# Optimization experiments

Hardware: AMD Instinct MI355X
Metric: run time of the kernel (lower is better)

Reference implementation:

```python
import jax, jax.numpy as jnp
import numpy as np

D_MODEL = 768
D_FF = 3072
N_EXPERTS = 4
BATCH, SEQ = 8, 2048


def setup_inputs() -> dict:
    key = jax.random.key(0)
    ks = jax.random.split(key, 8)
    s_in = 1.0 / np.sqrt(D_MODEL)
    s_ff = 1.0 / np.sqrt(D_FF)
    return {
        "hidden_states": jax.random.normal(ks[0], (BATCH, SEQ, D_MODEL), jnp.float32),
        "Wg": jax.random.normal(ks[1], (D_MODEL, N_EXPERTS), jnp.float32) * s_in,
        "bg": jnp.zeros((N_EXPERTS,), jnp.float32),
        "W1": jax.random.normal(ks[2], (N_EXPERTS, D_MODEL, D_FF), jnp.float32) * s_in,
        "b1": jnp.zeros((N_EXPERTS, D_FF), jnp.float32),
        "W2": jax.random.normal(ks[3], (N_EXPERTS, D_FF, D_MODEL), jnp.float32) * s_ff,
        "b2": jnp.zeros((N_EXPERTS, D_MODEL), jnp.float32),
    }


def reference(hidden_states, Wg, bg, W1, b1, W2, b2):
    """Switch-Transformer top-1 MoE FFN (no token dropping).

    router: softmax(x @ Wg + bg); each token goes to argmax expert,
    expert FFN: gelu(x @ W1[e] + b1[e]) @ W2[e] + b2[e],
    output scaled by the winning route probability.
    """
    B, S, D = hidden_states.shape
    xt = hidden_states.reshape(-1, D)                      # [T, D]
    logits = xt @ Wg + bg                                  # [T, E]
    probs = jax.nn.softmax(logits, axis=-1)
    gate = jnp.max(probs, axis=-1)                         # [T]
    route = jnp.argmax(probs, axis=-1)                     # [T] int

    out = jnp.zeros_like(xt)
    for e in range(W1.shape[0]):                           # small fixed expert count
        mask = (route == e).astype(xt.dtype)[:, None]      # [T, 1]
        h = jax.nn.gelu(xt @ W1[e] + b1[e])                # [T, d_ff]
        y = h @ W2[e] + b2[e]                              # [T, D]
        out = out + mask * y
    out = out * gate[:, None]
    return out.reshape(B, S, D)
```

## Files before the change

### kernel.cpp

```cpp
#include <hip/hip_runtime.h>
#include <hip/hip_bf16.h>

#define T_TOK 16384
#define DMODEL 768
#define DFF 3072
#define NEXP 4
#define ROWPAD 512
#define BK 64

typedef __attribute__((ext_vector_type(8))) short bf16x8;
typedef __attribute__((ext_vector_type(4))) float f32x4;

__device__ __forceinline__ void gl_lds16(const void* g, void* l) {
  __builtin_amdgcn_global_load_lds(
      (const __attribute__((address_space(1))) unsigned int*)g,
      (__attribute__((address_space(3))) unsigned int*)l, 16, 0, 0);
}

__device__ __forceinline__ short f2bf(float f) {
  union { float f; unsigned u; } v; v.f = f;
  unsigned r = v.u + 0x7fff + ((v.u >> 16) & 1);
  return (short)(r >> 16);
}

__device__ __forceinline__ float gelu_f(float x) {
  const float c = 0.7978845608028654f;
  float z = c * (x + 0.044715f * x * x * x);
  z = fminf(fmaxf(z, -15.f), 15.f);
  float e = __expf(-2.f * z);
  return 0.5f * x * (1.f + (1.f - e) / (1.f + e));
}


__device__ __forceinline__ int expert_aoff(const int* counts, int e) {
  int off = 0;
  for (int i = 0; i < e; ++i) off += (counts[i] + 127) & ~127;
  return off;
}

__global__ void route_kernel(const float* __restrict__ x, const float* __restrict__ Wg,
                             const float* __restrict__ bg, int* __restrict__ route,
                             float* __restrict__ gate) {
  int t = blockIdx.x * 4 + (threadIdx.x >> 6);
  int l = threadIdx.x & 63;
  const float* xr = x + (size_t)t * DMODEL;
  float s0 = 0.f, s1 = 0.f, s2 = 0.f, s3 = 0.f;
#pragma unroll
  for (int i = 0; i < DMODEL / 64; ++i) {
    int d = l + i * 64;
    float xv = xr[d];
    float4 w = *((const float4*)Wg + d);
    s0 += xv * w.x; s1 += xv * w.y; s2 += xv * w.z; s3 += xv * w.w;
  }
#pragma unroll
  for (int off = 32; off; off >>= 1) {
    s0 += __shfl_xor(s0, off);
    s1 += __shfl_xor(s1, off);
    s2 += __shfl_xor(s2, off);
    s3 += __shfl_xor(s3, off);
  }
  if (l == 0) {
    float lg[4] = { s0 + bg[0], s1 + bg[1], s2 + bg[2], s3 + bg[3] };
    int best = 0; float m = lg[0];
#pragma unroll
    for (int e = 1; e < 4; ++e) if (lg[e] > m) { m = lg[e]; best = e; }
    float s = 0.f;
#pragma unroll
    for (int e = 0; e < 4; ++e) s += __expf(lg[e] - m);
    route[t] = best;
    gate[t] = 1.0f / s;
  }
}

__global__ void bucket_kernel(const int* __restrict__ route, int* __restrict__ counts,
                              int* __restrict__ perm) {
  __shared__ int wcnt[4][NEXP];
  __shared__ int wpre[4][NEXP];
  __shared__ int base[NEXP];
  int tid = threadIdx.x;
  int t = blockIdx.x * 256 + tid;
  int w = tid >> 6, l = tid & 63;
  int r = route[t];
  int lanepre = 0;
  unsigned long long lower = (l == 0) ? 0ull : (~0ull >> (64 - l));
#pragma unroll
  for (int e = 0; e < NEXP; ++e) {
    unsigned long long m = __ballot(r == e);
    if (l == 0) wcnt[w][e] = (int)__popcll(m);
    if (r == e) lanepre = (int)__popcll(m & lower);
  }
  __syncthreads();
  if (tid < NEXP) {
    int s = 0;
#pragma unroll
    for (int ww = 0; ww < 4; ++ww) { wpre[ww][tid] = s; s += wcnt[ww][tid]; }
    base[tid] = atomicAdd(&counts[tid], s);
  }
  __syncthreads();
  int pos = base[r] + wpre[w][r] + lanepre;
  perm[r * T_TOK + pos] = t;
}

__global__ void gather_kernel(const float* __restrict__ x, const int* __restrict__ counts,
                              const int* __restrict__ perm, const float* __restrict__ gate,
                              short* __restrict__ xg, int* __restrict__ tokg,
                              float* __restrict__ gateg) {
  int e = blockIdx.y;
  int cnt = counts[e];
  int pos = blockIdx.x * 8 + (threadIdx.x >> 5);
  if (pos >= cnt) return;
  int off = expert_aoff(counts, e);
  int t = perm[e * T_TOK + pos];
  int g = off + pos;
  int l = threadIdx.x & 31;
  const float* src = x + (size_t)t * DMODEL;
  short* dst = xg + (size_t)g * DMODEL;
  int sw = g & 7;
#pragma unroll
  for (int i = 0; i < 3; ++i) {
    int c = l + 32 * i;
    float4 a = *((const float4*)src + c * 2);
    float4 b = *((const float4*)src + c * 2 + 1);
    bf16x8 v;
    v[0] = f2bf(a.x); v[1] = f2bf(a.y); v[2] = f2bf(a.z); v[3] = f2bf(a.w);
    v[4] = f2bf(b.x); v[5] = f2bf(b.y); v[6] = f2bf(b.z); v[7] = f2bf(b.w);
    int cs = (c & ~7) | ((c & 7) ^ sw);
    *(bf16x8*)(dst + cs * 8) = v;
  }
  if (l == 0) { tokg[g] = t; gateg[g] = gate[t]; }
}

__global__ void transpose_kernel(const float* __restrict__ src, short* __restrict__ dst,
                                 int K, int N) {
  __shared__ float lds[64 * 65];
  int e = blockIdx.z;
  int k0 = blockIdx.x * 64, n0 = blockIdx.y * 64;
  const float* s = src + (size_t)e * K * N;
  short* d = dst + (size_t)e * N * K;
#pragma unroll
  for (int i = 0; i < 16; ++i) {
    int idx = threadIdx.x + i * 256;
    int kk = idx >> 6, nn = idx & 63;
    lds[kk * 65 + nn] = s[(size_t)(k0 + kk) * N + n0 + nn];
  }
  __syncthreads();
#pragma unroll
  for (int i = 0; i < 2; ++i) {
    int cid = threadIdx.x + i * 256;
    int nn = cid >> 3, uu = cid & 7;
    int n = n0 + nn;
    bf16x8 v;
#pragma unroll
    for (int j = 0; j < 8; ++j) v[j] = f2bf(lds[(uu * 8 + j) * 65 + nn]);
    int cs = (k0 >> 3) + (uu ^ (n & 7));
    *(bf16x8*)(d + (size_t)n * K + cs * 8) = v;
  }
}

__device__ __forceinline__ int xcd_chunk(int orig, int nwg) {
  int q = nwg >> 3, r = nwg & 7, xcd = orig & 7;
  return (xcd < r ? xcd * (q + 1) : r * (q + 1) + (xcd - r) * q) + (orig >> 3);
}

__device__ __forceinline__ bool decode_expert(const int* counts, int gm,
                                              int& e, int& off, int& cnt, int& m0) {
  int c0 = counts[0], c1 = counts[1], c2 = counts[2], c3 = counts[3];
  int mb0 = (c0 + 127) >> 7, mb1 = (c1 + 127) >> 7, mb2 = (c2 + 127) >> 7, mb3 = (c3 + 127) >> 7;
  int o1 = (c0 + 127) & ~127, o2 = o1 + ((c1 + 127) & ~127), o3 = o2 + ((c2 + 127) & ~127);
  if (gm < mb0)                        { e = 0; off = 0;  cnt = c0; m0 = gm << 7; return true; }
  if (gm < mb0 + mb1)                  { e = 1; off = o1; cnt = c1; m0 = (gm - mb0) << 7; return true; }
  if (gm < mb0 + mb1 + mb2)            { e = 2; off = o2; cnt = c2; m0 = (gm - mb0 - mb1) << 7; return true; }
  if (gm < mb0 + mb1 + mb2 + mb3)      { e = 3; off = o3; cnt = c3; m0 = (gm - mb0 - mb1 - mb2) << 7; return true; }
  return false;
}

__global__ __launch_bounds__(256, 4)
void gemm1_kernel(const short* __restrict__ xg, const short* __restrict__ w1t,
                  const float* __restrict__ b1, const int* __restrict__ counts,
                  short* __restrict__ h, int FFC, int chunk, int MBG) {
  __shared__ __align__(16) short smem[2 * 128 * 64];
  short* sA = smem;
  short* sB = smem + 128 * 64;
  int L = xcd_chunk(blockIdx.x, gridDim.x);
  int np = L / MBG, gm = L - np * MBG;
  int e, off, cnt, m0;
  if (!decode_expert(counts, gm, e, off, cnt, m0)) return;
  int n0c = np * 128;
  int n0g = chunk * FFC + n0c;

  const char* Abase = (const char*)(xg + (size_t)(off + m0) * DMODEL);
  const char* Bbase = (const char*)(w1t + (size_t)e * DFF * DMODEL + (size_t)n0g * DMODEL);

  int tid = threadIdx.x, wid = tid >> 6, lane = tid & 63;
  int wm = wid >> 1, wn = wid & 1;
  int l15 = lane & 15, u4 = lane >> 4;

  f32x4 acc[4][4];
#pragma unroll
  for (int i = 0; i < 4; ++i)
#pragma unroll
    for (int j = 0; j < 4; ++j) acc[i][j] = (f32x4){0.f, 0.f, 0.f, 0.f};

  for (int kt = 0; kt < DMODEL / BK; ++kt) {
    int kb = kt * 128;
#pragma unroll
    for (int r = 0; r < 4; ++r) {
      int o = wid * 1024 + r * 4096 + lane * 16;
      int row = o >> 7, b = o & 127;
      gl_lds16(Abase + (size_t)row * (DMODEL * 2) + kb + b, (char*)sA + wid * 1024 + r * 4096);
      gl_lds16(Bbase + (size_t)row * (DMODEL * 2) + kb + b, (char*)sB + wid * 1024 + r * 4096);
    }
    __syncthreads();
#pragma unroll
    for (int ks = 0; ks < 2; ++ks) {
      int u = ks * 4 + u4;
      int slot8 = (u ^ (l15 & 7)) << 3;
      bf16x8 af[4], bfr[4];
#pragma unroll
      for (int mi = 0; mi < 4; ++mi)
        af[mi] = *(const bf16x8*)&sA[(wm * 64 + mi * 16 + l15) * 64 + slot8];
#pragma unroll
      for (int ni = 0; ni < 4; ++ni)
        bfr[ni] = *(const bf16x8*)&sB[(wn * 64 + ni * 16 + l15) * 64 + slot8];
#pragma unroll
      for (int mi = 0; mi < 4; ++mi)
#pragma unroll
        for (int ni = 0; ni < 4; ++ni)
          acc[mi][ni] = __builtin_amdgcn_mfma_f32_16x16x32_bf16(af[mi], bfr[ni], acc[mi][ni], 0, 0, 0);
    }
    __syncthreads();
  }

  float bbs[4];
#pragma unroll
  for (int ni = 0; ni < 4; ++ni) bbs[ni] = b1[e * DFF + n0g + wn * 64 + ni * 16 + l15];
  short* bounce = smem;
#pragma unroll
  for (int mi = 0; mi < 4; ++mi)
#pragma unroll
    for (int ni = 0; ni < 4; ++ni) {
      f32x4 v = acc[mi][ni];
      int col = wn * 64 + ni * 16 + l15;
      int c = col >> 3;
#pragma unroll
      for (int qq = 0; qq < 4; ++qq) {
        int rl = wm * 64 + mi * 16 + u4 * 4 + qq;
        int swc = (c & ~7) | ((c & 7) ^ (rl & 7));
        bounce[rl * 128 + swc * 8 + (col & 7)] = f2bf(gelu_f(v[qq] + bbs[ni]));
      }
    }
  __syncthreads();
#pragma unroll
  for (int it = 0; it < 8; ++it) {
    int cc = tid + it * 256;
    int rw = cc >> 4, sl = cc & 15;
    int grow = m0 + rw;
    if (grow < cnt) {
      size_t g = (size_t)off + grow;
      *(bf16x8*)((char*)h + (g * FFC + n0c) * 2 + sl * 16) =
          *(const bf16x8*)((char*)bounce + cc * 16);
    }
  }
}

__global__ __launch_bounds__(256, 4)
void gemm2_kernel(const short* __restrict__ h, const short* __restrict__ w2t,
                  const float* __restrict__ b2, const int* __restrict__ counts,
                  const int* __restrict__ tokg, const float* __restrict__ gateg,
                  float* __restrict__ out, int FFC, int chunk, int nchunks, int MBG) {
  __shared__ __align__(16) short sA[128 * 64];
  __shared__ __align__(16) short sB[128 * 64];
  int L = xcd_chunk(blockIdx.x, gridDim.x);
  int np = L / MBG, gm = L - np * MBG;
  int e, off, cnt, m0;
  if (!decode_expert(counts, gm, e, off, cnt, m0)) return;
  int n0 = np * 128;

  const char* Ar = (const char*)(h + (size_t)(off + m0) * FFC);
  const char* Br = (const char*)(w2t + (size_t)e * DMODEL * DFF + (size_t)n0 * DFF + (size_t)chunk * FFC);

  int tid = threadIdx.x, wid = tid >> 6, lane = tid & 63;
  int wm = wid >> 1, wn = wid & 1;
  int l15 = lane & 15, u4 = lane >> 4;

  f32x4 acc[4][4];
#pragma unroll
  for (int i = 0; i < 4; ++i)
#pragma unroll
    for (int j = 0; j < 4; ++j) acc[i][j] = (f32x4){0.f, 0.f, 0.f, 0.f};

  for (int kt = 0; kt < FFC / BK; ++kt) {
    int kb = kt * 128;
#pragma unroll
    for (int r = 0; r < 4; ++r) {
      int o = wid * 1024 + r * 4096 + lane * 16;
      int row = o >> 7, b = o & 127;
      gl_lds16(Ar + (size_t)row * (FFC * 2) + kb + b, (char*)sA + wid * 1024 + r * 4096);
      gl_lds16(Br + (size_t)row * (DFF * 2) + kb + b, (char*)sB + wid * 1024 + r * 4096);
    }
    __syncthreads();
#pragma unroll
    for (int ks = 0; ks < 2; ++ks) {
      int u = ks * 4 + u4;
      int slot8 = (u ^ (l15 & 7)) << 3;
      bf16x8 af[4], bfr[4];
#pragma unroll
      for (int mi = 0; mi < 4; ++mi)
        af[mi] = *(const bf16x8*)&sA[(wm * 64 + mi * 16 + l15) * 64 + slot8];
#pragma unroll
      for (int ni = 0; ni < 4; ++ni)
        bfr[ni] = *(const bf16x8*)&sB[(wn * 64 + ni * 16 + l15) * 64 + slot8];
#pragma unroll
      for (int mi = 0; mi < 4; ++mi)
#pragma unroll
        for (int ni = 0; ni < 4; ++ni)
          acc[mi][ni] = __builtin_amdgcn_mfma_f32_16x16x32_bf16(af[mi], bfr[ni], acc[mi][ni], 0, 0, 0);
    }
    __syncthreads();
  }

#pragma unroll
  for (int ni = 0; ni < 4; ++ni) {
    int colg = n0 + wn * 64 + ni * 16 + l15;
    float bb = b2[e * DMODEL + colg];
#pragma unroll
    for (int mi = 0; mi < 4; ++mi) {
      f32x4 v = acc[mi][ni];
#pragma unroll
      for (int qq = 0; qq < 4; ++qq) {
        int ml = m0 + wm * 64 + mi * 16 + u4 * 4 + qq;
        if (ml < cnt) {
          int g = off + ml;
          float* op = out + (size_t)tokg[g] * DMODEL + colg;
          float pv = v[qq];
          if (chunk == 0 && nchunks > 1) {
            *op = pv;
          } else if (chunk < nchunks - 1) {
            *op += pv;
          } else {
            float prev = (nchunks > 1) ? *op : 0.f;
            *op = (prev + pv + bb) * gateg[g];
          }
        }
      }
    }
  }
}

extern "C" void kernel_launch(void* const* d_in, const int* in_sizes, int n_in,
                              void* d_out, int out_size, void* d_ws, size_t ws_size,
                              hipStream_t stream) {
  (void)in_sizes; (void)n_in; (void)out_size;
  const float* x  = (const float*)d_in[0];
  const float* Wg = (const float*)d_in[1];
  const float* bg = (const float*)d_in[2];
  const float* W1 = (const float*)d_in[3];
  const float* b1 = (const float*)d_in[4];
  const float* W2 = (const float*)d_in[5];
  const float* b2 = (const float*)d_in[6];
  float* out = (float*)d_out;
  char* ws = (char*)d_ws;

  size_t cur = 0;
  auto take = [&](size_t bytes) -> size_t {
    cur = (cur + 255) & ~(size_t)255;
    size_t r = cur; cur += bytes; return r;
  };
  size_t o_counts = take(64);
  size_t o_perm  = take((size_t)NEXP * T_TOK * 4);
  size_t o_route = take((size_t)T_TOK * 4);
  size_t o_gate  = take((size_t)T_TOK * 4);
  size_t o_tokg  = take((size_t)(T_TOK + ROWPAD) * 4);
  size_t o_gateg = take((size_t)(T_TOK + ROWPAD) * 4);
  size_t o_w1t   = take((size_t)NEXP * DFF * DMODEL * 2);
  size_t o_w2t   = take((size_t)NEXP * DMODEL * DFF * 2);
  size_t o_xg    = take((size_t)(T_TOK + ROWPAD) * DMODEL * 2);
  cur = (cur + 255) & ~(size_t)255;
  size_t o_h = cur;

  int FFC = 384;
  const int cands[4] = {3072, 1536, 768, 384};
  for (int i = 0; i < 4; ++i) {
    if (o_h + (size_t)(T_TOK + ROWPAD) * cands[i] * 2 <= ws_size) { FFC = cands[i]; break; }
  }

  int*   counts = (int*)(ws + o_counts);
  int*   perm   = (int*)(ws + o_perm);
  int*   routeb = (int*)(ws + o_route);
  float* gate   = (float*)(ws + o_gate);
  int*   tokg   = (int*)(ws + o_tokg);
  float* gateg  = (float*)(ws + o_gateg);
  short* w1t    = (short*)(ws + o_w1t);
  short* w2t    = (short*)(ws + o_w2t);
  short* xg     = (short*)(ws + o_xg);
  short* hbuf   = (short*)(ws + o_h);

  hipMemsetAsync(counts, 0, 64, stream);
  route_kernel<<<T_TOK / 4, 256, 0, stream>>>(x, Wg, bg, routeb, gate);
  bucket_kernel<<<T_TOK / 256, 256, 0, stream>>>(routeb, counts, perm);
  transpose_kernel<<<dim3(DMODEL / 64, DFF / 64, NEXP), 256, 0, stream>>>(W1, w1t, DMODEL, DFF);
  transpose_kernel<<<dim3(DFF / 64, DMODEL / 64, NEXP), 256, 0, stream>>>(W2, w2t, DFF, DMODEL);
  gather_kernel<<<dim3(T_TOK / 8, NEXP), 256, 0, stream>>>(x, counts, perm, gate, xg, tokg, gateg);

  int NC = DFF / FFC;
  int MBG = T_TOK / 128 + (NEXP - 1);
  int NB2 = DMODEL / 128;
  for (int c = 0; c < NC; ++c) {
    int NB1 = FFC / 128;
    gemm1_kernel<<<NB1 * MBG, 256, 0, stream>>>(xg, w1t, b1, counts, hbuf, FFC, c, MBG);
    gemm2_kernel<<<NB2 * MBG, 256, 0, stream>>>(hbuf, w2t, b2, counts, tokg, gateg, out, FFC, c, NC, MBG);
  }
}
```

Baseline: 313.7 us.

## Double-buffer LDS tiles in both expert GEMM kernels to overlap loads with MFMA

Both gemm1 and gemm2 now keep two shared-memory buffers for the A and B tiles. The next K-tile is prefetched with global_load_lds while MFMAs run on the current one, which removes the load-then-wait stall each K step. This doubles LDS per block to 64KB, so launch bounds drop from 4 to 2 blocks per CU. Less cross-block latency hiding is traded for in-block overlap, and the register budget grows.

```diff
diff --git a/kernel.cpp b/kernel.cpp
--- a/kernel.cpp
+++ b/kernel.cpp
@@ -174,13 +174,12 @@
   return false;
 }
 
-__global__ __launch_bounds__(256, 4)
+__global__ __launch_bounds__(256, 2)
 void gemm1_kernel(const short* __restrict__ xg, const short* __restrict__ w1t,
                   const float* __restrict__ b1, const int* __restrict__ counts,
                   short* __restrict__ h, int FFC, int chunk, int MBG) {
-  __shared__ __align__(16) short smem[2 * 128 * 64];
-  short* sA = smem;
-  short* sB = smem + 128 * 64;
+  __shared__ __align__(16) short sA[2][128 * 64];
+  __shared__ __align__(16) short sB[2][128 * 64];
   int L = xcd_chunk(blockIdx.x, gridDim.x);
   int np = L / MBG, gm = L - np * MBG;
   int e, off, cnt, m0;
@@ -201,16 +200,23 @@
 #pragma unroll
     for (int j = 0; j < 4; ++j) acc[i][j] = (f32x4){0.f, 0.f, 0.f, 0.f};
 
-  for (int kt = 0; kt < DMODEL / BK; ++kt) {
-    int kb = kt * 128;
-#pragma unroll
-    for (int r = 0; r < 4; ++r) {
-      int o = wid * 1024 + r * 4096 + lane * 16;
-      int row = o >> 7, b = o & 127;
-      gl_lds16(Abase + (size_t)row * (DMODEL * 2) + kb + b, (char*)sA + wid * 1024 + r * 4096);
-      gl_lds16(Bbase + (size_t)row * (DMODEL * 2) + kb + b, (char*)sB + wid * 1024 + r * 4096);
-    }
-    __syncthreads();
+#define STG1(buf, kt) { int kb = (kt) * 128;                                       \
+    _Pragma("unroll")                                                              \
+    for (int r = 0; r < 4; ++r) {                                                  \
+      int o = wid * 1024 + r * 4096 + lane * 16;                                   \
+      int row = o >> 7, bo = o & 127;                                              \
+      gl_lds16(Abase + (size_t)row * (DMODEL * 2) + kb + bo,                       \
+               (char*)&sA[buf][0] + wid * 1024 + r * 4096);                        \
+      gl_lds16(Bbase + (size_t)row * (DMODEL * 2) + kb + bo,                       \
+               (char*)&sB[buf][0] + wid * 1024 + r * 4096);                        \
+    } }
+
+  const int KT = DMODEL / BK;
+  STG1(0, 0);
+  __syncthreads();
+  int cur = 0;
+  for (int kt = 0; kt < KT; ++kt) {
+    if (kt + 1 < KT) STG1(cur ^ 1, kt + 1);
 #pragma unroll
     for (int ks = 0; ks < 2; ++ks) {
       int u = ks * 4 + u4;
@@ -218,10 +224,10 @@
       bf16x8 af[4], bfr[4];
 #pragma unroll
       for (int mi = 0; mi < 4; ++mi)
-        af[mi] = *(const bf16x8*)&sA[(wm * 64 + mi * 16 + l15) * 64 + slot8];
+        af[mi] = *(const bf16x8*)&sA[cur][(wm * 64 + mi * 16 + l15) * 64 + slot8];
 #pragma unroll
       for (int ni = 0; ni < 4; ++ni)
-        bfr[ni] = *(const bf16x8*)&sB[(wn * 64 + ni * 16 + l15) * 64 + slot8];
+        bfr[ni] = *(const bf16x8*)&sB[cur][(wn * 64 + ni * 16 + l15) * 64 + slot8];
 #pragma unroll
       for (int mi = 0; mi < 4; ++mi)
 #pragma unroll
@@ -229,12 +235,14 @@
           acc[mi][ni] = __builtin_amdgcn_mfma_f32_16x16x32_bf16(af[mi], bfr[ni], acc[mi][ni], 0, 0, 0);
     }
     __syncthreads();
-  }
+    cur ^= 1;
+  }
+#undef STG1
 
   float bbs[4];
 #pragma unroll
   for (int ni = 0; ni < 4; ++ni) bbs[ni] = b1[e * DFF + n0g + wn * 64 + ni * 16 + l15];
-  short* bounce = smem;
+  short* bounce = &sA[0][0];
 #pragma unroll
   for (int mi = 0; mi < 4; ++mi)
 #pragma unroll
@@ -263,13 +271,13 @@
   }
 }
 
-__global__ __launch_bounds__(256, 4)
+__global__ __launch_bounds__(256, 2)
 void gemm2_kernel(const short* __restrict__ h, const short* __restrict__ w2t,
                   const float* __restrict__ b2, const int* __restrict__ counts,
                   const int* __restrict__ tokg, const float* __restrict__ gateg,
                   float* __restrict__ out, int FFC, int chunk, int nchunks, int MBG) {
-  __shared__ __align__(16) short sA[128 * 64];
-  __shared__ __align__(16) short sB[128 * 64];
+  __shared__ __align__(16) short sA[2][128 * 64];
+  __shared__ __align__(16) short sB[2][128 * 64];
   int L = xcd_chunk(blockIdx.x, gridDim.x);
   int np = L / MBG, gm = L - np * MBG;
   int e, off, cnt, m0;
@@ -289,16 +297,23 @@
 #pragma unroll
     for (int j = 0; j < 4; ++j) acc[i][j] = (f32x4){0.f, 0.f, 0.f, 0.f};
 
-  for (int kt = 0; kt < FFC / BK; ++kt) {
-    int kb = kt * 128;
-#pragma unroll
-    for (int r = 0; r < 4; ++r) {
-      int o = wid * 1024 + r * 4096 + lane * 16;
-      int row = o >> 7, b = o & 127;
-      gl_lds16(Ar + (size_t)row * (FFC * 2) + kb + b, (char*)sA + wid * 1024 + r * 4096);
-      gl_lds16(Br + (size_t)row * (DFF * 2) + kb + b, (char*)sB + wid * 1024 + r * 4096);
-    }
-    __syncthreads();
+#define STG2(buf, kt) { int kb = (kt) * 128;                                       \
+    _Pragma("unroll")                                                              \
+    for (int r = 0; r < 4; ++r) {                                                  \
+      int o = wid * 1024 + r * 4096 + lane * 16;                                   \
+      int row = o >> 7, bo = o & 127;                                              \
+      gl_lds16(Ar + (size_t)row * (FFC * 2) + kb + bo,                             \
+               (char*)&sA[buf][0] + wid * 1024 + r * 4096);                        \
+      gl_lds16(Br + (size_t)row * (DFF * 2) + kb + bo,                             \
+               (char*)&sB[buf][0] + wid * 1024 + r * 4096);                        \
+    } }
+
+  const int KT = FFC / BK;
+  STG2(0, 0);
+  __syncthreads();
+  int cur = 0;
+  for (int kt = 0; kt < KT; ++kt) {
+    if (kt + 1 < KT) STG2(cur ^ 1, kt + 1);
 #pragma unroll
     for (int ks = 0; ks < 2; ++ks) {
       int u = ks * 4 + u4;
@@ -306,10 +321,10 @@
       bf16x8 af[4], bfr[4];
 #pragma unroll
       for (int mi = 0; mi < 4; ++mi)
-        af[mi] = *(const bf16x8*)&sA[(wm * 64 + mi * 16 + l15) * 64 + slot8];
+        af[mi] = *(const bf16x8*)&sA[cur][(wm * 64 + mi * 16 + l15) * 64 + slot8];
 #pragma unroll
       for (int ni = 0; ni < 4; ++ni)
-        bfr[ni] = *(const bf16x8*)&sB[(wn * 64 + ni * 16 + l15) * 64 + slot8];
+        bfr[ni] = *(const bf16x8*)&sB[cur][(wn * 64 + ni * 16 + l15) * 64 + slot8];
 #pragma unroll
       for (int mi = 0; mi < 4; ++mi)
 #pragma unroll
@@ -317,7 +332,9 @@
           acc[mi][ni] = __builtin_amdgcn_mfma_f32_16x16x32_bf16(af[mi], bfr[ni], acc[mi][ni], 0, 0, 0);
     }
     __syncthreads();
-  }
+    cur ^= 1;
+  }
+#undef STG2
 
 #pragma unroll
   for (int ni = 0; ni < 4; ++ni) {
```

After: 365.8 us. 1.17x slower.
